# Performance work log

Measured on AMD Instinct MI355X. Metric: run time of the kernel, lower is better.

The kernel has to match this reference:

```python
import jax, jax.numpy as jnp
import numpy as np

H = 512  # hidden_dimension
B = 32
S = 2048


def setup_inputs() -> dict:
    key = jax.random.key(0)
    k1, k2, k3, k4, k5, k6 = jax.random.split(key, 6)
    decoder_hide = jax.random.normal(k1, (B, H), dtype=jnp.float32)
    encoder_out = jax.random.normal(k2, (B, S, 2 * H), dtype=jnp.float32)
    mask = jax.random.randint(k3, (B, S), 0, 2, dtype=jnp.int32)
    bound = 1.0 / np.sqrt(3 * H)
    W_attn = jax.random.uniform(k4, (3 * H, H), minval=-bound, maxval=bound, dtype=jnp.float32)
    b_attn = jax.random.uniform(k5, (H,), minval=-bound, maxval=bound, dtype=jnp.float32)
    bound_v = 1.0 / np.sqrt(H)
    v_w = jax.random.uniform(k6, (H,), minval=-bound_v, maxval=bound_v, dtype=jnp.float32)
    return {"decoder_hide": decoder_hide, "encoder_out": encoder_out, "mask": mask,
            "W_attn": W_attn, "b_attn": b_attn, "v_w": v_w}


def reference(decoder_hide, encoder_out, mask, W_attn, b_attn, v_w):
    # Split the concat-linear: cat((h, enc)) @ W == h @ W[:H] + enc @ W[H:]
    W_h = W_attn[:H]        # [H, H]
    W_e = W_attn[H:]        # [2H, H]
    dec_proj = decoder_hide @ W_h + b_attn                 # [B, H]
    enc_proj = jnp.einsum('bse,eh->bsh', encoder_out, W_e)  # [B, S, H]
    energy = jnp.tanh(enc_proj + dec_proj[:, None, :])      # [B, S, H]
    attention = jnp.einsum('bsh,h->bs', energy, v_w)        # [B, S]
    attention = jnp.where(mask == 0, jnp.float32(-100000.0), attention)
    return jax.nn.softmax(attention, axis=1)
```

## Files before the change

### kernel.cpp

```cpp
#include <hip/hip_runtime.h>
#include <math.h>

#define Hdim 512
#define Bdim 32
#define Sdim 2048
#define Kdim 1024
#define Mtot (Bdim * Sdim)

#define BM 128
#define BN 128
#define BK 32
#define AST 40

typedef __attribute__((ext_vector_type(8))) short short8;
typedef __attribute__((ext_vector_type(4))) float floatx4;

__device__ __forceinline__ short f2bf(float f) {
    union { float f; unsigned u; } v; v.f = f;
    unsigned r = v.u + 0x7fffu + ((v.u >> 16) & 1u);
    return (short)(r >> 16);
}

__device__ __forceinline__ float fast_tanh(float x) {
    float ax = fabsf(x);
    float e  = __expf(-2.0f * ax);
    float r  = (1.0f - e) / (1.0f + e);
    return copysignf(r, x);
}

__global__ __launch_bounds__(256) void conv_W_kernel(
    const float* __restrict__ W_attn, short* __restrict__ Wb)
{
    const float* We = W_attn + Hdim * Hdim;
    __shared__ short tile[32][33];
    const int k0 = (blockIdx.x >> 4) * 32;
    const int n0 = (blockIdx.x & 15) * 32;
    const int r = threadIdx.x >> 5, c = threadIdx.x & 31;
    #pragma unroll
    for (int rr = 0; rr < 4; ++rr)
        tile[r + rr * 8][c] = f2bf(We[(size_t)(k0 + r + rr * 8) * Hdim + n0 + c]);
    __syncthreads();
    #pragma unroll
    for (int rr = 0; rr < 4; ++rr)
        Wb[(size_t)(n0 + r + rr * 8) * Kdim + k0 + c] = tile[c][r + rr * 8];
}

__global__ __launch_bounds__(256) void dec_proj_kernel(
    const float* __restrict__ dec, const float* __restrict__ W_attn,
    const float* __restrict__ b_attn, float* __restrict__ dec_proj)
{
    __shared__ float part[2][128];
    const int b  = blockIdx.x;
    const int cb = blockIdx.y;
    const int t  = threadIdx.x;
    const int c  = cb * 128 + (t & 127);
    const int kh = t >> 7;
    float acc = 0.0f;
    const int kbeg = kh * 256, kend = kbeg + 256;
    #pragma unroll 8
    for (int k = kbeg; k < kend; ++k)
        acc = fmaf(dec[b * Hdim + k], W_attn[(size_t)k * Hdim + c], acc);
    part[kh][t & 127] = acc;
    __syncthreads();
    if (t < 128)
        dec_proj[b * Hdim + cb * 128 + t] = part[0][t] + part[1][t] + b_attn[cb * 128 + t];
}

__global__ __launch_bounds__(256, 3) void scores_kernel(
    const float* __restrict__ enc,
    const short* __restrict__ Wb,
    const float* __restrict__ dec_proj,
    const float* __restrict__ v_w,
    float* __restrict__ part)
{
    __shared__ __align__(16) short Asm[BM * AST];
    __shared__ __align__(16) short Bsm[BN * AST];
    __shared__ float redl[BM][2];

    const int t    = threadIdx.x;
    const int nblk = blockIdx.x & 3;
    const int mblk = blockIdx.x >> 2;
    const int row0 = mblk * BM;
    const int n0   = nblk * BN;
    const int b    = row0 / Sdim;

    const int w    = t >> 6;
    const int lane = t & 63;
    const int ln   = lane & 15;
    const int quad = lane >> 4;
    const int wr   = (w >> 1) * 64;
    const int wc   = (w & 1) * 64;

    const int sm = t >> 1;
    const int sk = (t & 1) * 16;

    floatx4 acc[4][4];
    #pragma unroll
    for (int i = 0; i < 4; ++i)
        #pragma unroll
        for (int j = 0; j < 4; ++j)
            acc[i][j] = (floatx4)(0.0f);

    const float* Ag = enc + (size_t)(row0 + sm) * Kdim + sk;
    const short* Bg = Wb + (size_t)(n0 + sm) * Kdim + sk;

    for (int kt = 0; kt < Kdim; kt += BK) {
        __syncthreads();
        {
            const floatx4* g = (const floatx4*)(Ag + kt);
            floatx4 f0 = g[0], f1 = g[1], f2 = g[2], f3 = g[3];
            short8 lo, hi;
            lo[0]=f2bf(f0.x); lo[1]=f2bf(f0.y); lo[2]=f2bf(f0.z); lo[3]=f2bf(f0.w);
            lo[4]=f2bf(f1.x); lo[5]=f2bf(f1.y); lo[6]=f2bf(f1.z); lo[7]=f2bf(f1.w);
            hi[0]=f2bf(f2.x); hi[1]=f2bf(f2.y); hi[2]=f2bf(f2.z); hi[3]=f2bf(f2.w);
            hi[4]=f2bf(f3.x); hi[5]=f2bf(f3.y); hi[6]=f2bf(f3.z); hi[7]=f2bf(f3.w);
            *(short8*)&Asm[sm * AST + sk]     = lo;
            *(short8*)&Asm[sm * AST + sk + 8] = hi;
        }
        {
            const short8* g = (const short8*)(Bg + kt);
            *(short8*)&Bsm[sm * AST + sk]     = g[0];
            *(short8*)&Bsm[sm * AST + sk + 8] = g[1];
        }
        __syncthreads();

        short8 af[4], bf[4];
        #pragma unroll
        for (int i = 0; i < 4; ++i)
            af[i] = *(const short8*)&Asm[(wr + i * 16 + ln) * AST + quad * 8];
        #pragma unroll
        for (int j = 0; j < 4; ++j)
            bf[j] = *(const short8*)&Bsm[(wc + j * 16 + ln) * AST + quad * 8];
        #pragma unroll
        for (int i = 0; i < 4; ++i)
            #pragma unroll
            for (int j = 0; j < 4; ++j)
                acc[i][j] = __builtin_amdgcn_mfma_f32_16x16x32_bf16(
                                af[i], bf[j], acc[i][j], 0, 0, 0);
    }

    float dpv[4], vwv[4];
    #pragma unroll
    for (int j = 0; j < 4; ++j) {
        int col = n0 + wc + j * 16 + ln;
        dpv[j] = dec_proj[b * Hdim + col];
        vwv[j] = v_w[col];
    }
    #pragma unroll
    for (int i = 0; i < 4; ++i) {
        #pragma unroll
        for (int reg = 0; reg < 4; ++reg) {
            float s = 0.0f;
            #pragma unroll
            for (int j = 0; j < 4; ++j) {
                float x = acc[i][j][reg] + dpv[j];
                s = fmaf(vwv[j], fast_tanh(x), s);
            }
            s += __shfl_xor(s, 1, 64);
            s += __shfl_xor(s, 2, 64);
            s += __shfl_xor(s, 4, 64);
            s += __shfl_xor(s, 8, 64);
            if (ln == 0)
                redl[wr + i * 16 + quad * 4 + reg][w & 1] = s;
        }
    }
    __syncthreads();
    if (t < BM)
        part[(size_t)nblk * Mtot + row0 + t] = redl[t][0] + redl[t][1];
}

__global__ __launch_bounds__(256) void softmax_kernel(
    const float* __restrict__ part, const int* __restrict__ mask,
    float* __restrict__ out)
{
    __shared__ float sred[8];
    const int b = blockIdx.x;
    const int t = threadIdx.x;
    const int lane = t & 63;
    const int wid  = t >> 6;

    float x[8];
    float m = -1e30f;
    #pragma unroll
    for (int j = 0; j < 8; ++j) {
        int idx = b * Sdim + j * 256 + t;
        float v = part[idx] + part[Mtot + idx] + part[2 * Mtot + idx] + part[3 * Mtot + idx];
        if (mask[idx] == 0) v = -100000.0f;
        x[j] = v;
        m = fmaxf(m, v);
    }
    #pragma unroll
    for (int off = 32; off >= 1; off >>= 1)
        m = fmaxf(m, __shfl_xor(m, off, 64));
    if (lane == 0) sred[wid] = m;
    __syncthreads();
    m = fmaxf(fmaxf(sred[0], sred[1]), fmaxf(sred[2], sred[3]));

    float s = 0.0f;
    #pragma unroll
    for (int j = 0; j < 8; ++j) {
        float e = __expf(x[j] - m);
        x[j] = e;
        s += e;
    }
    #pragma unroll
    for (int off = 32; off >= 1; off >>= 1)
        s += __shfl_xor(s, off, 64);
    if (lane == 0) sred[4 + wid] = s;
    __syncthreads();
    s = sred[4] + sred[5] + sred[6] + sred[7];

    const float inv = 1.0f / s;
    #pragma unroll
    for (int j = 0; j < 8; ++j)
        out[b * Sdim + j * 256 + t] = x[j] * inv;
}

extern "C" void kernel_launch(void* const* d_in, const int* in_sizes, int n_in,
                              void* d_out, int out_size, void* d_ws, size_t ws_size,
                              hipStream_t stream) {
    const float* dec  = (const float*)d_in[0];
    const float* enc  = (const float*)d_in[1];
    const int*   mask = (const int*)  d_in[2];
    const float* W    = (const float*)d_in[3];
    const float* ba   = (const float*)d_in[4];
    const float* vw   = (const float*)d_in[5];
    float* out = (float*)d_out;

    float* dec_proj = (float*)d_ws;
    short* Wb       = (short*)(dec_proj + Bdim * Hdim);
    float* part     = (float*)(Wb + Hdim * Kdim);

    conv_W_kernel<<<512, 256, 0, stream>>>(W, Wb);
    dec_proj_kernel<<<dim3(Bdim, 4), 256, 0, stream>>>(dec, W, ba, dec_proj);
    scores_kernel<<<(Mtot / BM) * 4, 256, 0, stream>>>(enc, Wb, dec_proj, vw, part);
    softmax_kernel<<<Bdim, 256, 0, stream>>>(part, mask, out);
}
```

Baseline: 486.3 us.

## Use direct global-to-LDS loads, XOR-swizzled LDS, BK=64, and merge prep kernels

The GEMM main loop now loads the bf16 weight tile straight into LDS with global_load_lds, which bypasses registers. Both LDS tiles use an XOR swizzle in place of padding, so that fragment reads avoid bank conflicts. The K tile grows to 64, halving the barrier count per K. Activation conversion uses packed bf16 intrinsics, and the weight-conversion and decoder-projection kernels are merged into one launch. The cost is more LDS per block, which may reduce occupancy, and reliance on correct swizzle indexing.

```diff
diff --git a/kernel.cpp b/kernel.cpp
--- a/kernel.cpp
+++ b/kernel.cpp
@@ -1,4 +1,5 @@
 #include <hip/hip_runtime.h>
+#include <hip/hip_bf16.h>
 #include <math.h>
 
 #define Hdim 512
@@ -9,8 +10,7 @@
 
 #define BM 128
 #define BN 128
-#define BK 32
-#define AST 40
+#define BK 64
 
 typedef __attribute__((ext_vector_type(8))) short short8;
 typedef __attribute__((ext_vector_type(4))) float floatx4;
@@ -19,6 +19,15 @@
     union { float f; unsigned u; } v; v.f = f;
     unsigned r = v.u + 0x7fffu + ((v.u >> 16) & 1u);
     return (short)(r >> 16);
+}
+
+__device__ __forceinline__ short8 cvt8(float4 a, float4 b) {
+    union { short8 s; __hip_bfloat162 h[4]; } u;
+    u.h[0] = __float22bfloat162_rn(make_float2(a.x, a.y));
+    u.h[1] = __float22bfloat162_rn(make_float2(a.z, a.w));
+    u.h[2] = __float22bfloat162_rn(make_float2(b.x, b.y));
+    u.h[3] = __float22bfloat162_rn(make_float2(b.z, b.w));
+    return u.s;
 }
 
 __device__ __forceinline__ float fast_tanh(float x) {
@@ -28,42 +37,42 @@
     return copysignf(r, x);
 }
 
-__global__ __launch_bounds__(256) void conv_W_kernel(
-    const float* __restrict__ W_attn, short* __restrict__ Wb)
+__global__ __launch_bounds__(256) void prep_kernel(
+    const float* __restrict__ W_attn, const float* __restrict__ dec,
+    const float* __restrict__ b_attn, short* __restrict__ Wb,
+    float* __restrict__ dec_proj)
 {
-    const float* We = W_attn + Hdim * Hdim;
-    __shared__ short tile[32][33];
-    const int k0 = (blockIdx.x >> 4) * 32;
-    const int n0 = (blockIdx.x & 15) * 32;
-    const int r = threadIdx.x >> 5, c = threadIdx.x & 31;
-    #pragma unroll
-    for (int rr = 0; rr < 4; ++rr)
-        tile[r + rr * 8][c] = f2bf(We[(size_t)(k0 + r + rr * 8) * Hdim + n0 + c]);
-    __syncthreads();
-    #pragma unroll
-    for (int rr = 0; rr < 4; ++rr)
-        Wb[(size_t)(n0 + r + rr * 8) * Kdim + k0 + c] = tile[c][r + rr * 8];
-}
-
-__global__ __launch_bounds__(256) void dec_proj_kernel(
-    const float* __restrict__ dec, const float* __restrict__ W_attn,
-    const float* __restrict__ b_attn, float* __restrict__ dec_proj)
-{
-    __shared__ float part[2][128];
-    const int b  = blockIdx.x;
-    const int cb = blockIdx.y;
-    const int t  = threadIdx.x;
-    const int c  = cb * 128 + (t & 127);
-    const int kh = t >> 7;
-    float acc = 0.0f;
-    const int kbeg = kh * 256, kend = kbeg + 256;
-    #pragma unroll 8
-    for (int k = kbeg; k < kend; ++k)
-        acc = fmaf(dec[b * Hdim + k], W_attn[(size_t)k * Hdim + c], acc);
-    part[kh][t & 127] = acc;
-    __syncthreads();
-    if (t < 128)
-        dec_proj[b * Hdim + cb * 128 + t] = part[0][t] + part[1][t] + b_attn[cb * 128 + t];
+    const int t = threadIdx.x;
+    if (blockIdx.x < 512) {
+        const float* We = W_attn + Hdim * Hdim;
+        __shared__ short tile[32][33];
+        const int k0 = (blockIdx.x >> 4) * 32;
+        const int n0 = (blockIdx.x & 15) * 32;
+        const int r = t >> 5, c = t & 31;
+        #pragma unroll
+        for (int rr = 0; rr < 4; ++rr)
+            tile[r + rr * 8][c] = f2bf(We[(size_t)(k0 + r + rr * 8) * Hdim + n0 + c]);
+        __syncthreads();
+        #pragma unroll
+        for (int rr = 0; rr < 4; ++rr)
+            Wb[(size_t)(n0 + r + rr * 8) * Kdim + k0 + c] = tile[c][r + rr * 8];
+    } else {
+        __shared__ float partl[2][128];
+        const int bid = blockIdx.x - 512;
+        const int b  = bid >> 2;
+        const int cb = bid & 3;
+        const int c  = cb * 128 + (t & 127);
+        const int kh = t >> 7;
+        float acc = 0.0f;
+        const int kbeg = kh * 256, kend = kbeg + 256;
+        #pragma unroll 8
+        for (int k = kbeg; k < kend; ++k)
+            acc = fmaf(dec[b * Hdim + k], W_attn[(size_t)k * Hdim + c], acc);
+        partl[kh][t & 127] = acc;
+        __syncthreads();
+        if (t < 128)
+            dec_proj[b * Hdim + cb * 128 + t] = partl[0][t] + partl[1][t] + b_attn[cb * 128 + t];
+    }
 }
 
 __global__ __launch_bounds__(256, 3) void scores_kernel(
@@ -73,8 +82,8 @@
     const float* __restrict__ v_w,
     float* __restrict__ part)
 {
-    __shared__ __align__(16) short Asm[BM * AST];
-    __shared__ __align__(16) short Bsm[BN * AST];
+    __shared__ __align__(16) short Asm[BM * BK];
+    __shared__ __align__(16) short Bsm[BN * BK];
     __shared__ float redl[BM][2];
 
     const int t    = threadIdx.x;
@@ -91,8 +100,31 @@
     const int wr   = (w >> 1) * 64;
     const int wc   = (w & 1) * 64;
 
-    const int sm = t >> 1;
-    const int sk = (t & 1) * 16;
+    const int sm  = t >> 1;
+    const int sh  = t & 1;
+    const int smx = sm & 7;
+    const float* Ag = enc + (size_t)(row0 + sm) * Kdim + sh * 32;
+    short* Aw = Asm + sm * BK;
+    int awc[4];
+    #pragma unroll
+    for (int i = 0; i < 4; ++i) awc[i] = ((sh * 4 + i) ^ smx) * 8;
+
+    const int l3 = lane >> 3, l7 = lane & 7;
+    int boff[4];
+    #pragma unroll
+    for (int r = 0; r < 4; ++r)
+        boff[r] = (n0 + (w * 4 + r) * 8 + l3) * Kdim + ((l7 ^ l3) * 8);
+    short* bbase = Bsm + w * 2048;
+
+    const int lnx = ln & 7;
+    int arow[4], brow[4];
+    #pragma unroll
+    for (int i = 0; i < 4; ++i) {
+        arow[i] = (wr + i * 16 + ln) * BK;
+        brow[i] = (wc + i * 16 + ln) * BK;
+    }
+    const int pf0 = ((0 * 4 + quad) ^ lnx) * 8;
+    const int pf1 = ((1 * 4 + quad) ^ lnx) * 8;
 
     floatx4 acc[4][4];
     #pragma unroll
@@ -101,42 +133,42 @@
         for (int j = 0; j < 4; ++j)
             acc[i][j] = (floatx4)(0.0f);
 
-    const float* Ag = enc + (size_t)(row0 + sm) * Kdim + sk;
-    const short* Bg = Wb + (size_t)(n0 + sm) * Kdim + sk;
-
     for (int kt = 0; kt < Kdim; kt += BK) {
         __syncthreads();
+        #pragma unroll
+        for (int r = 0; r < 4; ++r) {
+            const short* gp = Wb + boff[r] + kt;
+            __builtin_amdgcn_global_load_lds(
+                (const __attribute__((address_space(1))) unsigned int*)(const void*)gp,
+                (__attribute__((address_space(3))) unsigned int*)(void*)(bbase + r * 512),
+                16, 0, 0);
+        }
         {
-            const floatx4* g = (const floatx4*)(Ag + kt);
-            floatx4 f0 = g[0], f1 = g[1], f2 = g[2], f3 = g[3];
-            short8 lo, hi;
-            lo[0]=f2bf(f0.x); lo[1]=f2bf(f0.y); lo[2]=f2bf(f0.z); lo[3]=f2bf(f0.w);
-            lo[4]=f2bf(f1.x); lo[5]=f2bf(f1.y); lo[6]=f2bf(f1.z); lo[7]=f2bf(f1.w);
-            hi[0]=f2bf(f2.x); hi[1]=f2bf(f2.y); hi[2]=f2bf(f2.z); hi[3]=f2bf(f2.w);
-            hi[4]=f2bf(f3.x); hi[5]=f2bf(f3.y); hi[6]=f2bf(f3.z); hi[7]=f2bf(f3.w);
-            *(short8*)&Asm[sm * AST + sk]     = lo;
-            *(short8*)&Asm[sm * AST + sk + 8] = hi;
-        }
-        {
-            const short8* g = (const short8*)(Bg + kt);
-            *(short8*)&Bsm[sm * AST + sk]     = g[0];
-            *(short8*)&Bsm[sm * AST + sk + 8] = g[1];
-        }
-        __syncthreads();
-
-        short8 af[4], bf[4];
-        #pragma unroll
-        for (int i = 0; i < 4; ++i)
-            af[i] = *(const short8*)&Asm[(wr + i * 16 + ln) * AST + quad * 8];
-        #pragma unroll
-        for (int j = 0; j < 4; ++j)
-            bf[j] = *(const short8*)&Bsm[(wc + j * 16 + ln) * AST + quad * 8];
-        #pragma unroll
-        for (int i = 0; i < 4; ++i)
-            #pragma unroll
-            for (int j = 0; j < 4; ++j)
-                acc[i][j] = __builtin_amdgcn_mfma_f32_16x16x32_bf16(
-                                af[i], bf[j], acc[i][j], 0, 0, 0);
+            const float4* g = (const float4*)(Ag + kt);
+            float4 f0 = g[0], f1 = g[1], f2 = g[2], f3 = g[3];
+            float4 f4 = g[4], f5 = g[5], f6 = g[6], f7 = g[7];
+            *(short8*)&Aw[awc[0]] = cvt8(f0, f1);
+            *(short8*)&Aw[awc[1]] = cvt8(f2, f3);
+            *(short8*)&Aw[awc[2]] = cvt8(f4, f5);
+            *(short8*)&Aw[awc[3]] = cvt8(f6, f7);
+        }
+        __syncthreads();
+
+        #pragma unroll
+        for (int f = 0; f < 2; ++f) {
+            const int pf = f ? pf1 : pf0;
+            short8 af[4], bfr[4];
+            #pragma unroll
+            for (int i = 0; i < 4; ++i) af[i]  = *(const short8*)&Asm[arow[i] + pf];
+            #pragma unroll
+            for (int j = 0; j < 4; ++j) bfr[j] = *(const short8*)&Bsm[brow[j] + pf];
+            #pragma unroll
+            for (int i = 0; i < 4; ++i)
+                #pragma unroll
+                for (int j = 0; j < 4; ++j)
+                    acc[i][j] = __builtin_amdgcn_mfma_f32_16x16x32_bf16(
+                                    af[i], bfr[j], acc[i][j], 0, 0, 0);
+        }
     }
 
     float dpv[4], vwv[4];
@@ -231,8 +263,7 @@
     short* Wb       = (short*)(dec_proj + Bdim * Hdim);
     float* part     = (float*)(Wb + Hdim * Kdim);
 
-    conv_W_kernel<<<512, 256, 0, stream>>>(W, Wb);
-    dec_proj_kernel<<<dim3(Bdim, 4), 256, 0, stream>>>(dec, W, ba, dec_proj);
+    prep_kernel<<<640, 256, 0, stream>>>(W, dec, ba, Wb, dec_proj);
     scores_kernel<<<(Mtot / BM) * 4, 256, 0, stream>>>(enc, Wb, dec_proj, vw, part);
     softmax_kernel<<<Bdim, 256, 0, stream>>>(part, mask, out);
 }
```

Measured after the change: 489.0 us. About the same (+0.6%).
